# Kernel optimization log

Hardware: AMD Instinct MI355X
Metric: run time of the kernel (lower is better)

Reference implementation:

```python
import jax, jax.numpy as jnp
import numpy as np

B, N, Q, H = 32, 1024, 64, 768


def setup_inputs() -> dict:
    key = jax.random.key(0)
    k1, k2, k3, k4 = jax.random.split(key, 4)
    return {
        "nodes_compress": jax.random.normal(k1, (B, N, H), dtype=jnp.float32),
        "query_compress": jax.random.normal(k2, (B, Q, H), dtype=jnp.float32),
        "nodes_hidden": jax.random.normal(k3, (B, N, H), dtype=jnp.float32),
        # nn.Linear(3H, 1, bias=False).weight flattened to (3H,)
        "w": jax.random.normal(k4, (3 * H,), dtype=jnp.float32) * (1.0 / np.sqrt(3 * H)),
    }


def reference(nodes_compress, query_compress, nodes_hidden, w):
    h = nodes_compress.shape[-1]
    w_n, w_q, w_nq = w[:h], w[h:2 * h], w[2 * h:]
    # Decomposed trilinear similarity: identical to Linear([n, q, n*q]) -> scalar
    sim = (
        (nodes_compress @ w_n)[:, :, None]          # (B, N, 1)
        + (query_compress @ w_q)[:, None, :]        # (B, 1, Q)
        + jnp.einsum("bnh,bqh,h->bnq", nodes_compress, query_compress, w_nq)
    )                                                # (B, N, Q)
    # nodes -> query attention
    a = jax.nn.softmax(sim, axis=-1)                 # (B, N, Q)
    nodes2query = jnp.einsum("bnq,bqh->bnh", a, query_compress)
    # query -> nodes attention (max over query, softmax over nodes)
    b = jax.nn.softmax(jnp.max(sim, axis=-1), axis=-1)  # (B, N)
    q2n = jnp.einsum("bn,bnh->bh", b, nodes_compress)[:, None, :]  # (B, 1, H)
    q2n = jnp.broadcast_to(q2n, nodes_compress.shape)               # (B, N, H)
    return jnp.concatenate(
        [nodes_compress, nodes2query, nodes_compress * nodes2query, nodes_compress * q2n],
        axis=-1,
    )  # (B, N, 4H)
```

## Files before the change

### kernel.cpp

```cpp
#include <hip/hip_runtime.h>
#include <hip/hip_bf16.h>

#define BB 32
#define NN 1024
#define QQ 64
#define HH 768

typedef __attribute__((ext_vector_type(8))) short short8;
typedef __attribute__((ext_vector_type(4))) float f32x4;

#define GLOAD_LDS16(gp, lp) \
  __builtin_amdgcn_global_load_lds((const __attribute__((address_space(1))) unsigned int*)(gp), \
                                   (__attribute__((address_space(3))) unsigned int*)(lp), 16, 0, 0)

__device__ __forceinline__ unsigned short f2b(float f) {
  unsigned int u = __float_as_uint(f);
  unsigned int r = u + 0x7fffu + ((u >> 16) & 1u);
  return (unsigned short)(r >> 16);
}

__global__ void k_prep(const float* __restrict__ qc, const float* __restrict__ w,
                       unsigned short* __restrict__ qwB, unsigned short* __restrict__ qcT,
                       float* __restrict__ sq) {
  const int bid = blockIdx.x, tid = threadIdx.x;
  if (bid < 768) {
    int gid = bid * 256 + tid;
    int b = gid / 6144, rem = gid % 6144;
    int q = rem / 96, kk = rem % 96;
    int kc = kk >> 4, uu = kk & 15;
    const float* src = qc + ((size_t)(b * 64 + q) * HH + kk * 8);
    float4 g0 = *(const float4*)src, g1 = *(const float4*)(src + 4);
    int h = kk * 8;
    float4 n0 = *(const float4*)(w + h), n1 = *(const float4*)(w + h + 4);
    float4 m0 = *(const float4*)(w + 2 * HH + h), m1 = *(const float4*)(w + 2 * HH + h + 4);
    short8 v;
    v[0] = (short)f2b(g0.x * m0.x + n0.x); v[1] = (short)f2b(g0.y * m0.y + n0.y);
    v[2] = (short)f2b(g0.z * m0.z + n0.z); v[3] = (short)f2b(g0.w * m0.w + n0.w);
    v[4] = (short)f2b(g1.x * m1.x + n1.x); v[5] = (short)f2b(g1.y * m1.y + n1.y);
    v[6] = (short)f2b(g1.z * m1.z + n1.z); v[7] = (short)f2b(g1.w * m1.w + n1.w);
    size_t du = (size_t)(b * 6 + kc) * 1024 + q * 16 + (uu ^ (q & 7));
    *(short8*)((char*)qwB + du * 16) = v;
  } else if (bid < 1536) {
    int gid = (bid - 768) * 256 + tid;
    int b = gid / 6144, p = gid % 6144;
    int hc = p >> 10, pr = p & 1023, r = pr >> 3, x = pr & 7;
    int xu = x ^ (r & 7);
    int h = hc * 128 + r;
    const float* col = qc + ((size_t)(b * 64 + xu * 8) * HH + h);
    short8 v;
#pragma unroll
    for (int j = 0; j < 8; ++j) v[j] = (short)f2b(col[(size_t)j * HH]);
    *(short8*)((char*)qcT + (size_t)gid * 16) = v;
  } else {
    int wid = ((bid - 1536) * 256 + tid) >> 6;
    int l = tid & 63;
    const float* row = qc + (size_t)wid * HH;
    float s = 0.f;
#pragma unroll
    for (int i = 0; i < 12; ++i) s += row[i * 64 + l] * w[HH + i * 64 + l];
#pragma unroll
    for (int m = 1; m < 64; m <<= 1) s += __shfl_xor(s, m);
    if (l == 0) sq[wid] = s;
  }
}

__global__ __launch_bounds__(256) void k_sim(
    const float* __restrict__ nc, const unsigned short* __restrict__ qwB,
    const float* __restrict__ sq, float* __restrict__ partial,
    float* __restrict__ mtse, unsigned short* __restrict__ probs)
{
  __shared__ __align__(16) char bbuf[2][16384];
  __shared__ float rowmF[64];
  __shared__ float wvF[64];
  __shared__ float pW[4][768];

  const int tid = threadIdx.x;
  const int wv_ = tid >> 6, l = tid & 63;
  const int l15 = l & 15, lg = l >> 4;
  const int lb = (blockIdx.x & 7) * 64 + (blockIdx.x >> 3);
  const int b = lb >> 4, tile = lb & 15;
  const int row0 = tile * 64;

  const float* ncB = nc + (size_t)(b * NN + row0) * HH;
  const char* qwb = (const char*)qwB + (size_t)b * 98304;
  const float* aBase = ncB + (wv_ * 16 + l15) * HH + lg * 8;

  {
    const char* gsrc = qwb + wv_ * 4096 + l * 16;
#pragma unroll
    for (int i = 0; i < 4; ++i)
      GLOAD_LDS16(gsrc + i * 1024, &bbuf[0][wv_ * 4096 + i * 1024]);
  }
  float4 fr[2][8];
#pragma unroll
  for (int ks = 0; ks < 4; ++ks) {
    fr[0][ks * 2]     = *(const float4*)(aBase + ks * 32);
    fr[0][ks * 2 + 1] = *(const float4*)(aBase + ks * 32 + 4);
  }

  f32x4 acc[4] = {};
#pragma unroll
  for (int kc = 0; kc < 6; ++kc) {
    short8 af[4];
#pragma unroll
    for (int ks = 0; ks < 4; ++ks) {
      float4 f0 = fr[kc & 1][ks * 2], f1 = fr[kc & 1][ks * 2 + 1];
      short8 v;
      v[0] = (short)f2b(f0.x); v[1] = (short)f2b(f0.y);
      v[2] = (short)f2b(f0.z); v[3] = (short)f2b(f0.w);
      v[4] = (short)f2b(f1.x); v[5] = (short)f2b(f1.y);
      v[6] = (short)f2b(f1.z); v[7] = (short)f2b(f1.w);
      af[ks] = v;
    }
    if (kc < 5) {
#pragma unroll
      for (int ks = 0; ks < 4; ++ks) {
        fr[(kc + 1) & 1][ks * 2]     = *(const float4*)(aBase + (kc + 1) * 128 + ks * 32);
        fr[(kc + 1) & 1][ks * 2 + 1] = *(const float4*)(aBase + (kc + 1) * 128 + ks * 32 + 4);
      }
      const char* gsrc = qwb + (kc + 1) * 16384 + wv_ * 4096 + l * 16;
#pragma unroll
      for (int i = 0; i < 4; ++i)
        GLOAD_LDS16(gsrc + i * 1024, &bbuf[(kc + 1) & 1][wv_ * 4096 + i * 1024]);
      asm volatile("s_waitcnt vmcnt(12)" ::: "memory");
    } else {
      asm volatile("s_waitcnt vmcnt(0)" ::: "memory");
    }
    __builtin_amdgcn_s_barrier();
    __builtin_amdgcn_sched_barrier(0);
#pragma unroll
    for (int ks = 0; ks < 4; ++ks) {
      int kbyte = ks * 64 + lg * 16;
#pragma unroll
      for (int nt = 0; nt < 4; ++nt) {
        int brow = nt * 16 + l15;
        short8 bf = *(short8*)(&bbuf[kc & 1][0] + brow * 256 + (kbyte ^ ((l & 7) << 4)));
        acc[nt] = __builtin_amdgcn_mfma_f32_16x16x32_bf16(af[ks], bf, acc[nt], 0, 0, 0);
      }
    }
    __builtin_amdgcn_sched_barrier(0);
    __builtin_amdgcn_s_barrier();
  }

  unsigned short* pT = probs + (size_t)(b * 16 + tile) * (QQ * QQ);
  float sqv[4];
#pragma unroll
  for (int nt = 0; nt < 4; ++nt) sqv[nt] = sq[b * QQ + nt * 16 + l15];
#pragma unroll
  for (int j = 0; j < 4; ++j) {
    float mm = -1e30f;
#pragma unroll
    for (int nt = 0; nt < 4; ++nt) { acc[nt][j] += sqv[nt]; mm = fmaxf(mm, acc[nt][j]); }
    mm = fmaxf(mm, __shfl_xor(mm, 1));
    mm = fmaxf(mm, __shfl_xor(mm, 2));
    mm = fmaxf(mm, __shfl_xor(mm, 4));
    mm = fmaxf(mm, __shfl_xor(mm, 8));
    float ss = 0.f;
#pragma unroll
    for (int nt = 0; nt < 4; ++nt) { float p = __expf(acc[nt][j] - mm); acc[nt][j] = p; ss += p; }
    ss += __shfl_xor(ss, 1); ss += __shfl_xor(ss, 2);
    ss += __shfl_xor(ss, 4); ss += __shfl_xor(ss, 8);
    float inv = 1.0f / ss;
    int r = wv_ * 16 + lg * 4 + j;
#pragma unroll
    for (int nt = 0; nt < 4; ++nt)
      pT[r * 64 + nt * 16 + l15] = f2b(acc[nt][j] * inv);
    if (l15 == 0) rowmF[r] = mm;
  }
  __syncthreads();

  float m_t = -1e30f;
#pragma unroll
  for (int i = 0; i < 16; ++i) {
    f32x4 v = ((f32x4*)rowmF)[i];
    m_t = fmaxf(m_t, fmaxf(fmaxf(v[0], v[1]), fmaxf(v[2], v[3])));
  }
  if (tid < 64) wvF[tid] = __expf(rowmF[tid] - m_t);
  __syncthreads();
  {
    float sv = wvF[l];
#pragma unroll
    for (int m = 1; m < 64; m <<= 1) sv += __shfl_xor(sv, m);
    if (tid == 0) {
      mtse[(b * 16 + tile) * 2] = m_t;
      mtse[(b * 16 + tile) * 2 + 1] = sv;
    }
  }
  {
    float a[12];
#pragma unroll
    for (int j = 0; j < 12; ++j) a[j] = 0.f;
    for (int n0 = 0; n0 < 16; ++n0) {
      int n = wv_ * 16 + n0;
      float wvv = wvF[n];
      const float* pr = ncB + (size_t)n * HH;
#pragma unroll
      for (int j = 0; j < 12; ++j) a[j] += wvv * pr[l + j * 64];
    }
#pragma unroll
    for (int j = 0; j < 12; ++j) pW[wv_][l + j * 64] = a[j];
  }
  __syncthreads();
  {
    float* pp = partial + (size_t)(b * 16 + tile) * HH + tid;
    pp[0]   = pW[0][tid]       + pW[1][tid]       + pW[2][tid]       + pW[3][tid];
    pp[256] = pW[0][tid + 256] + pW[1][tid + 256] + pW[2][tid + 256] + pW[3][tid + 256];
    pp[512] = pW[0][tid + 512] + pW[1][tid + 512] + pW[2][tid + 512] + pW[3][tid + 512];
  }
}

__global__ __launch_bounds__(256) void k_out(
    const float* __restrict__ nc, const unsigned short* __restrict__ qcT,
    const unsigned short* __restrict__ probs, const float* __restrict__ partial,
    const float* __restrict__ mtse, float* __restrict__ out)
{
  __shared__ __align__(16) char smem[16384];
  __shared__ float q2nL[128];

  const int tid = threadIdx.x;
  const int wv_ = tid >> 6, l = tid & 63;
  const int l15 = l & 15, lg = l >> 4;
  const int lb = (blockIdx.x & 7) * 384 + (blockIdx.x >> 3);
  const int hc = lb % 6;
  const int bt = lb / 6;
  const int b = bt >> 4, tile = bt & 15;
  const int row0 = tile * 64;

  {
    const char* src = (const char*)qcT + ((size_t)(b * 6 + hc) << 14) + wv_ * 4096 + l * 16;
#pragma unroll
    for (int i = 0; i < 4; ++i)
      GLOAD_LDS16(src + i * 1024, &smem[wv_ * 4096 + i * 1024]);
  }

  if (tid < 128) {
    float M = -1e30f, mt[16], se[16];
#pragma unroll
    for (int i = 0; i < 16; ++i) {
      mt[i] = mtse[(b * 16 + i) * 2];
      se[i] = mtse[(b * 16 + i) * 2 + 1];
      M = fmaxf(M, mt[i]);
    }
    float denom = 0.f;
#pragma unroll
    for (int i = 0; i < 16; ++i) { mt[i] = __expf(mt[i] - M); denom += mt[i] * se[i]; }
    float inv = 1.0f / denom;
    float a = 0.f;
#pragma unroll
    for (int i = 0; i < 16; ++i)
      a += mt[i] * partial[(size_t)(b * 16 + i) * HH + hc * 128 + tid];
    q2nL[tid] = a * inv;
  }

  const unsigned short* pT = probs + (size_t)bt * (QQ * QQ);
  short8 a2_0 = *(const short8*)((const char*)pT + (wv_ * 16 + l15) * 128 + lg * 16);
  short8 a2_1 = *(const short8*)((const char*)pT + (wv_ * 16 + l15) * 128 + 64 + lg * 16);

  asm volatile("s_waitcnt vmcnt(0)" ::: "memory");
  __syncthreads();

  const int n = wv_ * 16 + l15;
  const float* ncrow = nc + (size_t)(b * NN + row0 + n) * HH;
  float* orow = out + (size_t)(b * NN + row0 + n) * 3072;

#pragma unroll
  for (int hg = 0; hg < 8; ++hg) {
    f32x4 c2 = {};
#pragma unroll
    for (int ks2 = 0; ks2 < 2; ++ks2) {
      int hrow = hg * 16 + l15;
      int kbyte = ks2 * 64 + lg * 16;
      short8 hf = *(short8*)(&smem[0] + hrow * 128 + (kbyte ^ ((l & 7) << 4)));
      c2 = __builtin_amdgcn_mfma_f32_16x16x32_bf16(hf, ks2 ? a2_1 : a2_0, c2, 0, 0, 0);
    }
    int hl = hg * 16 + lg * 4;
    int hbase = hc * 128 + hl;
    f32x4 ncv = *(const f32x4*)(ncrow + hbase);
    f32x4 qv  = *(const f32x4*)(&q2nL[hl]);
    *(f32x4*)(orow + hbase)          = ncv;
    *(f32x4*)(orow + HH + hbase)     = c2;
    *(f32x4*)(orow + 2 * HH + hbase) = ncv * c2;
    *(f32x4*)(orow + 2304 + hbase)   = ncv * qv;
  }
}

extern "C" void kernel_launch(void* const* d_in, const int* in_sizes, int n_in,
                              void* d_out, int out_size, void* d_ws, size_t ws_size,
                              hipStream_t stream) {
  (void)in_sizes; (void)n_in; (void)out_size; (void)ws_size;
  const float* nc = (const float*)d_in[0];
  const float* qc = (const float*)d_in[1];
  const float* w  = (const float*)d_in[3];
  float* out = (float*)d_out;
  char* ws = (char*)d_ws;
  unsigned short* qwB = (unsigned short*)(ws);
  unsigned short* qcT = (unsigned short*)(ws + 3145728);
  float* sqv     = (float*)(ws + 6291456);
  float* partial = (float*)(ws + 6299648);
  float* mtse    = (float*)(ws + 7872512);
  unsigned short* probs = (unsigned short*)(ws + 7876608);

  k_prep<<<2048, 256, 0, stream>>>(qc, w, qwB, qcT, sqv);
  k_sim<<<512, 256, 0, stream>>>(nc, qwB, sqv, partial, mtse, probs);
  k_out<<<3072, 256, 0, stream>>>(nc, qcT, probs, partial, mtse, out);
}
```

Baseline: 157.4 us.

## Restructure query prep to stage tiles in LDS and emit partial query dot sums

The prep kernel now has one block per (batch, 128-column chunk). Each block loads a 64x128 query tile into shared memory once and produces the scaled bf16 query operand, the transposed bf16 copy and per-chunk partial sums for the query-weight dot product. This replaces three separate block ranges that each re-read the query from global memory, including a strided column gather for the transpose. k_sim now adds the six partial sums itself. The launch drops from 2048 blocks to 192, so the GPU has far fewer blocks to spread across its compute units.

```diff
diff --git a/kernel.cpp b/kernel.cpp
--- a/kernel.cpp
+++ b/kernel.cpp
@@ -19,54 +19,71 @@
   return (unsigned short)(r >> 16);
 }
 
-__global__ void k_prep(const float* __restrict__ qc, const float* __restrict__ w,
-                       unsigned short* __restrict__ qwB, unsigned short* __restrict__ qcT,
-                       float* __restrict__ sq) {
-  const int bid = blockIdx.x, tid = threadIdx.x;
-  if (bid < 768) {
-    int gid = bid * 256 + tid;
-    int b = gid / 6144, rem = gid % 6144;
-    int q = rem / 96, kk = rem % 96;
-    int kc = kk >> 4, uu = kk & 15;
-    const float* src = qc + ((size_t)(b * 64 + q) * HH + kk * 8);
-    float4 g0 = *(const float4*)src, g1 = *(const float4*)(src + 4);
-    int h = kk * 8;
-    float4 n0 = *(const float4*)(w + h), n1 = *(const float4*)(w + h + 4);
-    float4 m0 = *(const float4*)(w + 2 * HH + h), m1 = *(const float4*)(w + 2 * HH + h + 4);
-    short8 v;
-    v[0] = (short)f2b(g0.x * m0.x + n0.x); v[1] = (short)f2b(g0.y * m0.y + n0.y);
-    v[2] = (short)f2b(g0.z * m0.z + n0.z); v[3] = (short)f2b(g0.w * m0.w + n0.w);
-    v[4] = (short)f2b(g1.x * m1.x + n1.x); v[5] = (short)f2b(g1.y * m1.y + n1.y);
-    v[6] = (short)f2b(g1.z * m1.z + n1.z); v[7] = (short)f2b(g1.w * m1.w + n1.w);
-    size_t du = (size_t)(b * 6 + kc) * 1024 + q * 16 + (uu ^ (q & 7));
-    *(short8*)((char*)qwB + du * 16) = v;
-  } else if (bid < 1536) {
-    int gid = (bid - 768) * 256 + tid;
-    int b = gid / 6144, p = gid % 6144;
-    int hc = p >> 10, pr = p & 1023, r = pr >> 3, x = pr & 7;
-    int xu = x ^ (r & 7);
-    int h = hc * 128 + r;
-    const float* col = qc + ((size_t)(b * 64 + xu * 8) * HH + h);
-    short8 v;
-#pragma unroll
-    for (int j = 0; j < 8; ++j) v[j] = (short)f2b(col[(size_t)j * HH]);
-    *(short8*)((char*)qcT + (size_t)gid * 16) = v;
-  } else {
-    int wid = ((bid - 1536) * 256 + tid) >> 6;
-    int l = tid & 63;
-    const float* row = qc + (size_t)wid * HH;
+__global__ __launch_bounds__(256) void k_prep(
+    const float* __restrict__ qc, const float* __restrict__ w,
+    unsigned short* __restrict__ qwB, unsigned short* __restrict__ qcT,
+    float* __restrict__ sq_part) {
+  __shared__ float qcL[128][66];
+
+  const int tid = threadIdx.x;
+  const int bid = blockIdx.x;
+  const int b = bid / 6, hc = bid % 6;
+  const float* qcB = qc + (size_t)(b * 64) * HH + hc * 128;
+
+#pragma unroll
+  for (int i = 0; i < 8; ++i) {
+    int u = i * 256 + tid;
+    int q = u >> 5, c4 = u & 31;
+    float4 v = *(const float4*)(qcB + (size_t)q * HH + c4 * 4);
+    qcL[c4 * 4 + 0][q] = v.x;
+    qcL[c4 * 4 + 1][q] = v.y;
+    qcL[c4 * 4 + 2][q] = v.z;
+    qcL[c4 * 4 + 3][q] = v.w;
+  }
+  __syncthreads();
+
+  {
+    char* dst = (char*)qwB + ((size_t)bid << 14);
+#pragma unroll
+    for (int i = 0; i < 4; ++i) {
+      int p = i * 256 + tid;
+      int q = p >> 4, uu = p & 15;
+      int hg = hc * 128 + uu * 8;
+      short8 v;
+#pragma unroll
+      for (int j = 0; j < 8; ++j)
+        v[j] = (short)f2b(qcL[uu * 8 + j][q] * w[2 * HH + hg + j] + w[hg + j]);
+      *(short8*)(dst + ((size_t)(q * 16 + (uu ^ (q & 7)))) * 16) = v;
+    }
+  }
+  {
+    char* dst = (char*)qcT + ((size_t)bid << 14);
+#pragma unroll
+    for (int i = 0; i < 4; ++i) {
+      int p = i * 256 + tid;
+      int r = p >> 3, x = p & 7;
+      int xu = x ^ (r & 7);
+      short8 v;
+#pragma unroll
+      for (int j = 0; j < 8; ++j) v[j] = (short)f2b(qcL[r][xu * 8 + j]);
+      *(short8*)(dst + (size_t)p * 16) = v;
+    }
+  }
+  {
+    int q = tid >> 2, qt = tid & 3;
     float s = 0.f;
 #pragma unroll
-    for (int i = 0; i < 12; ++i) s += row[i * 64 + l] * w[HH + i * 64 + l];
-#pragma unroll
-    for (int m = 1; m < 64; m <<= 1) s += __shfl_xor(s, m);
-    if (l == 0) sq[wid] = s;
+    for (int k = 0; k < 32; ++k)
+      s += qcL[qt * 32 + k][q] * w[HH + hc * 128 + qt * 32 + k];
+    s += __shfl_xor(s, 1);
+    s += __shfl_xor(s, 2);
+    if (qt == 0) sq_part[bid * 64 + q] = s;
   }
 }
 
 __global__ __launch_bounds__(256) void k_sim(
     const float* __restrict__ nc, const unsigned short* __restrict__ qwB,
-    const float* __restrict__ sq, float* __restrict__ partial,
+    const float* __restrict__ sq_part, float* __restrict__ partial,
     float* __restrict__ mtse, unsigned short* __restrict__ probs)
 {
   __shared__ __align__(16) char bbuf[2][16384];
@@ -145,7 +162,12 @@
   unsigned short* pT = probs + (size_t)(b * 16 + tile) * (QQ * QQ);
   float sqv[4];
 #pragma unroll
-  for (int nt = 0; nt < 4; ++nt) sqv[nt] = sq[b * QQ + nt * 16 + l15];
+  for (int nt = 0; nt < 4; ++nt) {
+    float s = 0.f;
+#pragma unroll
+    for (int i = 0; i < 6; ++i) s += sq_part[(b * 6 + i) * 64 + nt * 16 + l15];
+    sqv[nt] = s;
+  }
 #pragma unroll
   for (int j = 0; j < 4; ++j) {
     float mm = -1e30f;
@@ -295,12 +317,12 @@
   char* ws = (char*)d_ws;
   unsigned short* qwB = (unsigned short*)(ws);
   unsigned short* qcT = (unsigned short*)(ws + 3145728);
-  float* sqv     = (float*)(ws + 6291456);
-  float* partial = (float*)(ws + 6299648);
-  float* mtse    = (float*)(ws + 7872512);
-  unsigned short* probs = (unsigned short*)(ws + 7876608);
-
-  k_prep<<<2048, 256, 0, stream>>>(qc, w, qwB, qcT, sqv);
-  k_sim<<<512, 256, 0, stream>>>(nc, qwB, sqv, partial, mtse, probs);
+  float* sq_part = (float*)(ws + 6291456);
+  float* partial = (float*)(ws + 6340608);
+  float* mtse    = (float*)(ws + 7913472);
+  unsigned short* probs = (unsigned short*)(ws + 7917568);
+
+  k_prep<<<192, 256, 0, stream>>>(qc, w, qwB, qcT, sq_part);
+  k_sim<<<512, 256, 0, stream>>>(nc, qwB, sq_part, partial, mtse, probs);
   k_out<<<3072, 256, 0, stream>>>(nc, qcT, probs, partial, mtse, out);
 }
```

New measurement: 158.7 us. About the same (+0.8%).
